# Performance work log

Measured on AMD Instinct MI355X. Metric: run time of the kernel, lower is better.

Reference implementation:

```python
import jax, jax.numpy as jnp
import numpy as np

CELL = 128
STEPS = 20
N_KEYS = 4   # ['first_conn','second_conn','first_op','second_op']
N_OUT = 6


def setup_inputs() -> dict:
    key = jax.random.key(0)
    ks = jax.random.split(key, 10)
    s = 0.05
    return {
        "net": jax.random.randint(ks[0], (STEPS,), 0, N_OUT),          # sampled actions, each in [0,6)
        "reward": jax.random.uniform(ks[1], (1,), dtype=jnp.float32),   # unused in forward (kept for signature parity)
        "emb_start": jax.random.normal(ks[2], (1, CELL), jnp.float32) * s,          # Embedding(1,128)
        "emb_keys": jax.random.normal(ks[3], (N_KEYS, N_OUT, CELL), jnp.float32) * s,
        "fc_W": jax.random.normal(ks[4], (N_KEYS, N_OUT, CELL), jnp.float32) * s,
        "fc_b": jax.random.normal(ks[5], (N_KEYS, N_OUT), jnp.float32) * s,
        "W_ih": jax.random.normal(ks[6], (4 * CELL, CELL), jnp.float32) * s,  # LSTMCell input weights (i,f,g,o)
        "W_hh": jax.random.normal(ks[7], (4 * CELL, CELL), jnp.float32) * s,  # LSTMCell hidden weights
        "b_ih": jax.random.normal(ks[8], (4 * CELL,), jnp.float32) * s,
        "b_hh": jax.random.normal(ks[9], (4 * CELL,), jnp.float32) * s,
    }


def _lstm_cell(x, h, c, W_ih, W_hh, b_ih, b_hh):
    # PyTorch LSTMCell: gates ordered (i, f, g, o)
    gates = x @ W_ih.T + b_ih + h @ W_hh.T + b_hh   # [1, 4*CELL]
    i, f, g, o = jnp.split(gates, 4, axis=-1)
    c_new = jax.nn.sigmoid(f) * c + jax.nn.sigmoid(i) * jnp.tanh(g)
    h_new = jax.nn.sigmoid(o) * jnp.tanh(c_new)
    return h_new, c_new


def reference(net, reward, emb_start, emb_keys, fc_W, fc_b, W_ih, W_hh, b_ih, b_hh):
    key_idx = jnp.arange(STEPS) % N_KEYS            # which head/embedding at each step
    fc_W_t = fc_W[key_idx]                          # [STEPS, 6, CELL]
    fc_b_t = fc_b[key_idx]                          # [STEPS, 6]
    emb_t = emb_keys[key_idx, net]                  # [STEPS, CELL] next-step input embedding

    def step(carry, xs):
        h, c, x = carry
        Wt, bt, ev = xs
        h, c = _lstm_cell(x, h, c, W_ih, W_hh, b_ih, b_hh)
        probs = jax.nn.softmax(h @ Wt.T + bt, axis=1)   # [1, 6]
        return (h, c, ev[None, :]), probs

    h0 = jnp.zeros((1, CELL), dtype=emb_start.dtype)
    c0 = jnp.zeros((1, CELL), dtype=emb_start.dtype)
    x0 = emb_start                                   # embedding lookup of action 0 in a 1-row table
    _, outputs = jax.lax.scan(step, (h0, c0, x0), (fc_W_t, fc_b_t, emb_t))
    return outputs                                   # [STEPS, 1, 6], stacked version of the torch list
```

## Files before the change

### kernel.cpp

```cpp
#include <hip/hip_runtime.h>
#include <hip/hip_fp16.h>

#define CELL 128
#define STEPS 20

typedef _Float16 half8_t __attribute__((ext_vector_type(8)));
typedef float    floatx4 __attribute__((ext_vector_type(4)));

__device__ __forceinline__ unsigned packf2(float x, float y) {
    typedef _Float16 h2 __attribute__((ext_vector_type(2)));
    h2 h = { (_Float16)x, (_Float16)y };
    return __builtin_bit_cast(unsigned, h);
}
__device__ __forceinline__ float fdot2u(unsigned a, unsigned b, float c) {
    typedef _Float16 h2 __attribute__((ext_vector_type(2)));
#if __has_builtin(__builtin_amdgcn_fdot2)
    return __builtin_amdgcn_fdot2(__builtin_bit_cast(h2, a), __builtin_bit_cast(h2, b), c, false);
#else
    h2 x = __builtin_bit_cast(h2, a), y = __builtin_bit_cast(h2, b);
    return fmaf((float)x[0], (float)y[0], fmaf((float)x[1], (float)y[1], c));
#endif
}
__device__ __forceinline__ float fastrcp(float x) {
#if __has_builtin(__builtin_amdgcn_rcpf)
    return __builtin_amdgcn_rcpf(x);
#else
    return 1.0f / x;
#endif
}
__device__ __forceinline__ half8_t cvt8(const float* p) {
    const float4* p4 = (const float4*)p;
    float4 a = p4[0], b = p4[1];
    return half8_t{ (_Float16)a.x, (_Float16)a.y, (_Float16)a.z, (_Float16)a.w,
                    (_Float16)b.x, (_Float16)b.y, (_Float16)b.z, (_Float16)b.w };
}

extern "C" __global__ void __launch_bounds__(512, 1)
nas_policy_kernel(const int* __restrict__ net,
                  const float* __restrict__ emb_start,
                  const float* __restrict__ emb_keys,
                  const float* __restrict__ fc_W,
                  const float* __restrict__ fc_b,
                  const float* __restrict__ W_ih,
                  const float* __restrict__ W_hh,
                  const float* __restrict__ b_ih,
                  const float* __restrict__ b_hh,
                  float* __restrict__ out)
{
    const int t0   = threadIdx.x;
    const int wv   = t0 >> 6;
    const int lane = t0 & 63;
    const int quad = lane >> 4;
    const int lcol = lane & 15;

    __shared__ __align__(16) unsigned s_xv2[32 * 68];
    __shared__ __align__(16) float    s_gx[STEPS * 512];
    __shared__ __align__(16) unsigned hbuf[2 * 64];
    __shared__ unsigned s_fcw2[24 * 64];
    __shared__ float    s_fcb[24];
    __shared__ float    llog[STEPS * 8];

    for (int i = t0; i < STEPS * 64; i += 512) {
        const int m = i >> 6, j = i & 63;
        const float2* src = (m == 0) ? (const float2*)emb_start
            : (const float2*)(emb_keys + ((((m - 1) & 3) * 6) + net[m - 1]) * CELL);
        float2 v = src[j];
        s_xv2[m * 68 + j] = packf2(v.x, v.y);
    }
    {
        const float2* fw2 = (const float2*)fc_W;
        for (int i = t0; i < 24 * 64; i += 512) { float2 w = fw2[i]; s_fcw2[i] = packf2(w.x, w.y); }
    }
    if (t0 < 24) s_fcb[t0] = fc_b[t0];
    if (t0 < 64) hbuf[64 + t0] = 0u;

    const int rr0 = (wv << 4) + lcol;
    float biasx[4];
#pragma unroll
    for (int tau = 0; tau < 4; ++tau) {
        const int r = tau * 128 + rr0;
        biasx[tau] = b_ih[r] + b_hh[r];
    }

    __syncthreads();

    {
        half8_t bw[4][4];
#pragma unroll
        for (int kc = 0; kc < 4; ++kc) {
            const int k0 = kc * 32 + quad * 8;
#pragma unroll
            for (int tau = 0; tau < 4; ++tau)
                bw[kc][tau] = cvt8(W_ih + (tau * 128 + rr0) * CELL + k0);
        }
        floatx4 ax0[4] = { {0,0,0,0}, {0,0,0,0}, {0,0,0,0}, {0,0,0,0} };
        floatx4 ax1[4] = { {0,0,0,0}, {0,0,0,0}, {0,0,0,0}, {0,0,0,0} };
#pragma unroll
        for (int kc = 0; kc < 4; ++kc) {
            uint4 u0 = *(const uint4*)&s_xv2[lcol * 68 + kc * 16 + quad * 4];
            uint4 u1 = *(const uint4*)&s_xv2[(16 + lcol) * 68 + kc * 16 + quad * 4];
            half8_t a0f = __builtin_bit_cast(half8_t, u0);
            half8_t a1f = __builtin_bit_cast(half8_t, u1);
#pragma unroll
            for (int tau = 0; tau < 4; ++tau) {
                ax0[tau] = __builtin_amdgcn_mfma_f32_16x16x32_f16(a0f, bw[kc][tau], ax0[tau], 0, 0, 0);
                ax1[tau] = __builtin_amdgcn_mfma_f32_16x16x32_f16(a1f, bw[kc][tau], ax1[tau], 0, 0, 0);
            }
        }
#pragma unroll
        for (int tau = 0; tau < 4; ++tau) {
            const int r = tau * 128 + rr0;
#pragma unroll
            for (int reg = 0; reg < 4; ++reg)
                s_gx[(quad * 4 + reg) * 512 + r] = ax0[tau][reg] + biasx[tau];
            if (quad == 0) {
#pragma unroll
                for (int reg = 0; reg < 4; ++reg)
                    s_gx[(16 + reg) * 512 + r] = ax1[tau][reg] + biasx[tau];
            }
        }
    }

    half8_t bf0[4], bf1[4], bf2[4], bf3[4];
#pragma unroll
    for (int kc = 0; kc < 4; ++kc) {
        const int k0 = kc * 32 + quad * 8;
        bf0[kc] = cvt8(W_hh + (0 * 128 + rr0) * CELL + k0);
        bf1[kc] = cvt8(W_hh + (1 * 128 + rr0) * CELL + k0);
        bf2[kc] = cvt8(W_hh + (2 * 128 + rr0) * CELL + k0);
        bf3[kc] = cvt8(W_hh + (3 * 128 + rr0) * CELL + k0);
    }

    const float ascale = (quad == 2) ? 2.0f : 1.0f;
    const float amul   = (quad == 2) ? 2.0f : 1.0f;
    const float aadd   = (quad == 2) ? -1.0f : 0.0f;

    float c = 0.0f;
    __syncthreads();

    for (int t = 0; t < STEPS; ++t) {
        const uint4* hp4 = (const uint4*)(hbuf + (((t + 1) & 1) << 6));
        floatx4 a0a = {0,0,0,0}, a0b = {0,0,0,0}, a1a = {0,0,0,0}, a1b = {0,0,0,0};
        floatx4 a2a = {0,0,0,0}, a2b = {0,0,0,0}, a3a = {0,0,0,0}, a3b = {0,0,0,0};
        {
            uint4 u0 = hp4[(0 << 2) + quad], u1 = hp4[(1 << 2) + quad];
            uint4 u2 = hp4[(2 << 2) + quad], u3 = hp4[(3 << 2) + quad];
            half8_t f0 = __builtin_bit_cast(half8_t, u0), f1 = __builtin_bit_cast(half8_t, u1);
            half8_t f2 = __builtin_bit_cast(half8_t, u2), f3 = __builtin_bit_cast(half8_t, u3);
            a0a = __builtin_amdgcn_mfma_f32_16x16x32_f16(f0, bf0[0], a0a, 0, 0, 0);
            a1a = __builtin_amdgcn_mfma_f32_16x16x32_f16(f0, bf1[0], a1a, 0, 0, 0);
            a2a = __builtin_amdgcn_mfma_f32_16x16x32_f16(f0, bf2[0], a2a, 0, 0, 0);
            a3a = __builtin_amdgcn_mfma_f32_16x16x32_f16(f0, bf3[0], a3a, 0, 0, 0);
            a0b = __builtin_amdgcn_mfma_f32_16x16x32_f16(f1, bf0[1], a0b, 0, 0, 0);
            a1b = __builtin_amdgcn_mfma_f32_16x16x32_f16(f1, bf1[1], a1b, 0, 0, 0);
            a2b = __builtin_amdgcn_mfma_f32_16x16x32_f16(f1, bf2[1], a2b, 0, 0, 0);
            a3b = __builtin_amdgcn_mfma_f32_16x16x32_f16(f1, bf3[1], a3b, 0, 0, 0);
            a0a = __builtin_amdgcn_mfma_f32_16x16x32_f16(f2, bf0[2], a0a, 0, 0, 0);
            a1a = __builtin_amdgcn_mfma_f32_16x16x32_f16(f2, bf1[2], a1a, 0, 0, 0);
            a2a = __builtin_amdgcn_mfma_f32_16x16x32_f16(f2, bf2[2], a2a, 0, 0, 0);
            a3a = __builtin_amdgcn_mfma_f32_16x16x32_f16(f2, bf3[2], a3a, 0, 0, 0);
            a0b = __builtin_amdgcn_mfma_f32_16x16x32_f16(f3, bf0[3], a0b, 0, 0, 0);
            a1b = __builtin_amdgcn_mfma_f32_16x16x32_f16(f3, bf1[3], a1b, 0, 0, 0);
            a2b = __builtin_amdgcn_mfma_f32_16x16x32_f16(f3, bf2[3], a2b, 0, 0, 0);
            a3b = __builtin_amdgcn_mfma_f32_16x16x32_f16(f3, bf3[3], a3b, 0, 0, 0);
        }

        if (t >= 1 && wv < 6 && quad == 1) {
            const int li = lane & 15;
            const int hg = ((t - 1) & 3) * 6 + wv;
            const unsigned* hb = hbuf + (((t + 1) & 1) << 6);
            const unsigned* wp = s_fcw2 + hg * 64 + li * 4;
            float p = fdot2u(hb[li * 4],     wp[0], 0.0f);
            p = fdot2u(hb[li * 4 + 1], wp[1], p);
            p = fdot2u(hb[li * 4 + 2], wp[2], p);
            p = fdot2u(hb[li * 4 + 3], wp[3], p);
            p += __shfl_down(p, 8); p += __shfl_down(p, 4);
            p += __shfl_down(p, 2); p += __shfl_down(p, 1);
            if (li == 0) llog[(t - 1) * 8 + wv] = p + s_fcb[hg];
        }

        float gsum = (quad == 0) ? (a0a[0] + a0b[0])
                   : (quad == 1) ? (a1a[0] + a1b[0])
                   : (quad == 2) ? (a2a[0] + a2b[0])
                   :               (a3a[0] + a3b[0]);
        float u = gsum + s_gx[t * 512 + quad * 128 + rr0];
        float act = fmaf(amul, fastrcp(1.0f + __expf(-ascale * u)), aadd);

        float fg = __shfl(act, lane + 16);
        float gg = __shfl(act, lane + 32);
        float og = __shfl(act, lane + 48);
        if (lane < 16) {
            c = fg * c + act * gg;
            float th = fmaf(2.0f, fastrcp(1.0f + __expf(-2.0f * c)), -1.0f);
            float h = og * th;
            float hpv = __shfl_xor(h, 1);
            if ((lane & 1) == 0)
                hbuf[((t & 1) << 6) + (wv << 3) + (lane >> 1)] = packf2(h, hpv);
        }

        __syncthreads();
    }

    if (wv < 6 && quad == 1) {
        const int li = lane & 15;
        const int hg = (19 & 3) * 6 + wv;
        const unsigned* hb = hbuf + 64;
        const unsigned* wp = s_fcw2 + hg * 64 + li * 4;
        float p = fdot2u(hb[li * 4],     wp[0], 0.0f);
        p = fdot2u(hb[li * 4 + 1], wp[1], p);
        p = fdot2u(hb[li * 4 + 2], wp[2], p);
        p = fdot2u(hb[li * 4 + 3], wp[3], p);
        p += __shfl_down(p, 8); p += __shfl_down(p, 4);
        p += __shfl_down(p, 2); p += __shfl_down(p, 1);
        if (li == 0) llog[19 * 8 + wv] = p + s_fcb[hg];
    }
    __syncthreads();
    if (t0 < STEPS * 6) {
        const int s = t0 / 6, k = t0 - s * 6;
        const float* L = llog + s * 8;
        float l0 = L[0], l1 = L[1], l2 = L[2], l3 = L[3], l4 = L[4], l5 = L[5];
        float m = fmaxf(fmaxf(fmaxf(l0, l1), fmaxf(l2, l3)), fmaxf(l4, l5));
        float e0 = __expf(l0 - m), e1 = __expf(l1 - m), e2 = __expf(l2 - m);
        float e3 = __expf(l3 - m), e4 = __expf(l4 - m), e5 = __expf(l5 - m);
        float sum = ((e0 + e1) + (e2 + e3)) + (e4 + e5);
        float mine = (k == 0) ? e0 : (k == 1) ? e1 : (k == 2) ? e2
                   : (k == 3) ? e3 : (k == 4) ? e4 : e5;
        out[t0] = mine / sum;
    }
}

extern "C" void kernel_launch(void* const* d_in, const int* in_sizes, int n_in,
                              void* d_out, int out_size, void* d_ws, size_t ws_size,
                              hipStream_t stream) {
    (void)in_sizes; (void)n_in; (void)out_size; (void)d_ws; (void)ws_size;
    const int*   net       = (const int*)d_in[0];
    const float* emb_start = (const float*)d_in[2];
    const float* emb_keys  = (const float*)d_in[3];
    const float* fc_W      = (const float*)d_in[4];
    const float* fc_b      = (const float*)d_in[5];
    const float* W_ih      = (const float*)d_in[6];
    const float* W_hh      = (const float*)d_in[7];
    const float* b_ih      = (const float*)d_in[8];
    const float* b_hh      = (const float*)d_in[9];
    float*       out       = (float*)d_out;

    hipLaunchKernelGGL(nas_policy_kernel, dim3(1), dim3(512), 0, stream,
                       net, emb_start, emb_keys, fc_W, fc_b,
                       W_ih, W_hh, b_ih, b_hh, out);
}
```

Before: 99.40 us.

## Compute all four LSTM gates per lane and interleave gate precompute layout

Reorders the precomputed input-gate buffer so each hidden unit's four gate values are contiguous, letting each lane load them with one vector read. Each lane now evaluates all four gate activations itself instead of one gate per quad followed by three cross-lane shuffles. The hidden state is stored directly as fp16 per element rather than packed after a shuffle. This removes shuffle latency from the serial recurrence critical path, at the cost of more transcendental work per lane.

Result: no change. 98.76 us (-0.6%).

```diff
diff --git a/kernel.cpp b/kernel.cpp
--- a/kernel.cpp
+++ b/kernel.cpp
@@ -27,6 +27,12 @@
 #else
     return 1.0f / x;
 #endif
+}
+__device__ __forceinline__ float sig_rcp(float x) {
+    return fastrcp(1.0f + __expf(-x));
+}
+__device__ __forceinline__ float tanh_rcp(float x) {
+    return fmaf(2.0f, fastrcp(1.0f + __expf(-2.0f * x)), -1.0f);
 }
 __device__ __forceinline__ half8_t cvt8(const float* p) {
     const float4* p4 = (const float4*)p;
@@ -53,9 +59,9 @@
     const int quad = lane >> 4;
     const int lcol = lane & 15;
 
-    __shared__ __align__(16) unsigned s_xv2[32 * 68];
-    __shared__ __align__(16) float    s_gx[STEPS * 512];
-    __shared__ __align__(16) unsigned hbuf[2 * 64];
+    __shared__ __align__(16) unsigned  s_xv2[32 * 68];
+    __shared__ __align__(16) float     s_gx[STEPS * 512];
+    __shared__ __align__(16) _Float16  hbuf[2 * 128];
     __shared__ unsigned s_fcw2[24 * 64];
     __shared__ float    s_fcb[24];
     __shared__ float    llog[STEPS * 8];
@@ -71,8 +77,8 @@
         const float2* fw2 = (const float2*)fc_W;
         for (int i = t0; i < 24 * 64; i += 512) { float2 w = fw2[i]; s_fcw2[i] = packf2(w.x, w.y); }
     }
-    if (t0 < 24) s_fcb[t0] = fc_b[t0];
-    if (t0 < 64) hbuf[64 + t0] = 0u;
+    if (t0 < 24)  s_fcb[t0] = fc_b[t0];
+    if (t0 < 128) hbuf[128 + t0] = (_Float16)0.0f;
 
     const int rr0 = (wv << 4) + lcol;
     float biasx[4];
@@ -109,14 +115,13 @@
         }
 #pragma unroll
         for (int tau = 0; tau < 4; ++tau) {
-            const int r = tau * 128 + rr0;
 #pragma unroll
             for (int reg = 0; reg < 4; ++reg)
-                s_gx[(quad * 4 + reg) * 512 + r] = ax0[tau][reg] + biasx[tau];
+                s_gx[(quad * 4 + reg) * 512 + rr0 * 4 + tau] = ax0[tau][reg] + biasx[tau];
             if (quad == 0) {
 #pragma unroll
                 for (int reg = 0; reg < 4; ++reg)
-                    s_gx[(16 + reg) * 512 + r] = ax1[tau][reg] + biasx[tau];
+                    s_gx[(16 + reg) * 512 + rr0 * 4 + tau] = ax1[tau][reg] + biasx[tau];
             }
         }
     }
@@ -131,15 +136,12 @@
         bf3[kc] = cvt8(W_hh + (3 * 128 + rr0) * CELL + k0);
     }
 
-    const float ascale = (quad == 2) ? 2.0f : 1.0f;
-    const float amul   = (quad == 2) ? 2.0f : 1.0f;
-    const float aadd   = (quad == 2) ? -1.0f : 0.0f;
-
     float c = 0.0f;
     __syncthreads();
 
     for (int t = 0; t < STEPS; ++t) {
-        const uint4* hp4 = (const uint4*)(hbuf + (((t + 1) & 1) << 6));
+        const uint4* hp4 = (const uint4*)(hbuf + (((t + 1) & 1) << 7));
+        floatx4 gx = *(const floatx4*)&s_gx[t * 512 + rr0 * 4];
         floatx4 a0a = {0,0,0,0}, a0b = {0,0,0,0}, a1a = {0,0,0,0}, a1b = {0,0,0,0};
         floatx4 a2a = {0,0,0,0}, a2b = {0,0,0,0}, a3a = {0,0,0,0}, a3b = {0,0,0,0};
         {
@@ -166,9 +168,9 @@
         }
 
         if (t >= 1 && wv < 6 && quad == 1) {
-            const int li = lane & 15;
+            const int li = lcol;
             const int hg = ((t - 1) & 3) * 6 + wv;
-            const unsigned* hb = hbuf + (((t + 1) & 1) << 6);
+            const unsigned* hb = (const unsigned*)(hbuf + (((t + 1) & 1) << 7));
             const unsigned* wp = s_fcw2 + hg * 64 + li * 4;
             float p = fdot2u(hb[li * 4],     wp[0], 0.0f);
             p = fdot2u(hb[li * 4 + 1], wp[1], p);
@@ -179,32 +181,24 @@
             if (li == 0) llog[(t - 1) * 8 + wv] = p + s_fcb[hg];
         }
 
-        float gsum = (quad == 0) ? (a0a[0] + a0b[0])
-                   : (quad == 1) ? (a1a[0] + a1b[0])
-                   : (quad == 2) ? (a2a[0] + a2b[0])
-                   :               (a3a[0] + a3b[0]);
-        float u = gsum + s_gx[t * 512 + quad * 128 + rr0];
-        float act = fmaf(amul, fastrcp(1.0f + __expf(-ascale * u)), aadd);
-
-        float fg = __shfl(act, lane + 16);
-        float gg = __shfl(act, lane + 32);
-        float og = __shfl(act, lane + 48);
-        if (lane < 16) {
-            c = fg * c + act * gg;
-            float th = fmaf(2.0f, fastrcp(1.0f + __expf(-2.0f * c)), -1.0f);
-            float h = og * th;
-            float hpv = __shfl_xor(h, 1);
-            if ((lane & 1) == 0)
-                hbuf[((t & 1) << 6) + (wv << 3) + (lane >> 1)] = packf2(h, hpv);
+        {
+            float ig = sig_rcp (a0a[0] + a0b[0] + gx[0]);
+            float fg = sig_rcp (a1a[0] + a1b[0] + gx[1]);
+            float gg = tanh_rcp(a2a[0] + a2b[0] + gx[2]);
+            float og = sig_rcp (a3a[0] + a3b[0] + gx[3]);
+            c = fg * c + ig * gg;
+            float h = og * tanh_rcp(c);
+            if (quad == 0)
+                hbuf[((t & 1) << 7) + rr0] = (_Float16)h;
         }
 
         __syncthreads();
     }
 
     if (wv < 6 && quad == 1) {
-        const int li = lane & 15;
+        const int li = lcol;
         const int hg = (19 & 3) * 6 + wv;
-        const unsigned* hb = hbuf + 64;
+        const unsigned* hb = (const unsigned*)(hbuf + 128);
         const unsigned* wp = s_fcw2 + hg * 64 + li * 4;
         float p = fdot2u(hb[li * 4],     wp[0], 0.0f);
         p = fdot2u(hb[li * 4 + 1], wp[1], p);
```
